# Kernel optimization log

Hardware: AMD Instinct MI355X
Metric: run time of the kernel (lower is better)

## Reference

```python
import jax, jax.numpy as jnp
import numpy as np

B, T, R = 512, 4096, 16


def setup_inputs() -> dict:
    key = jax.random.key(0)
    k1, k2, k3 = jax.random.split(key, 3)
    pred = jax.random.normal(k1, (B, T, R), dtype=jnp.float32)
    target = jax.random.normal(k2, (B, T, R), dtype=jnp.float32)
    # replicate_mask marks a contiguous prefix of valid replicates (matches
    # the original `pred[b, :, :n_valid]` slicing). Lengths in [0, R].
    lengths = jax.random.randint(k3, (B,), 0, R + 1)
    replicate_mask = (jnp.arange(R)[None, :] < lengths[:, None]).astype(jnp.float32)
    return {"pred": pred, "target": target, "replicate_mask": replicate_mask}


def _masked_var_unbiased(x, m, n_safe):
    # x: [B,T,R], m: [B,1,R], n_safe: [B,1] (clamped >= 2)
    mean = jnp.sum(x * m, axis=-1, keepdims=True) / n_safe[:, :, None]  # [B,T,1]
    sq = jnp.sum(((x - mean) ** 2) * m, axis=-1)  # [B,T]
    return sq / (n_safe - 1.0)  # unbiased (torch var default ddof=1)


def reference(pred, target, replicate_mask):
    weight = 0.1
    n = jnp.sum(replicate_mask, axis=-1)  # [B]
    n_safe = jnp.maximum(n, 2.0)[:, None]  # avoid div-by-zero; masked out below
    m = replicate_mask[:, None, :]  # [B,1,R]
    pred_var = _masked_var_unbiased(pred, m, n_safe)      # [B,T]
    target_var = _masked_var_unbiased(target, m, n_safe)  # [B,T]
    mse = jnp.mean((pred_var - target_var) ** 2, axis=-1)  # [B]
    valid = n > 1.0
    n_multi = jnp.sum(valid.astype(jnp.float32))
    total = jnp.sum(jnp.where(valid, mse, 0.0))
    loss = jnp.where(n_multi > 0, total / jnp.maximum(n_multi, 1.0), 0.0)
    return weight * loss
```

## Files before the change

### kernel.cpp

```cpp
#include <hip/hip_runtime.h>

#define B_DIM 512
#define T_DIM 4096
#define NSLOT 256
#define THREADS 256
#define ITER 8
#define QROWS (B_DIM * T_DIM * 4)
#define BLOCKS (QROWS / (THREADS * ITER))

__device__ __forceinline__ float hsum4(float4 v) { return (v.x + v.y) + (v.z + v.w); }

__device__ __forceinline__ float mdot(float4 x, float4 m) {
    return (x.x * m.x + x.y * m.y) + (x.z * m.z + x.w * m.w);
}

__device__ __forceinline__ float mdot2(float4 x, float4 m) {
    return (x.x * x.x * m.x + x.y * x.y * m.y) + (x.z * x.z * m.z + x.w * x.w * m.w);
}

__device__ __forceinline__ float qsum(float v) {
    int t = __builtin_amdgcn_update_dpp(0, __float_as_int(v), 0xB1, 0xF, 0xF, true);
    v += __int_as_float(t);
    t = __builtin_amdgcn_update_dpp(0, __float_as_int(v), 0x4E, 0xF, 0xF, true);
    v += __int_as_float(t);
    return v;
}

__global__ __launch_bounds__(THREADS, 4) void rcl_main(
    const float4* __restrict__ pred4, const float4* __restrict__ targ4,
    const float4* __restrict__ mask4, double* __restrict__ slots)
{
    const int tid  = threadIdx.x;
    const int b    = blockIdx.x >> 3;
    const int base = blockIdx.x * (THREADS * ITER);

    const float4 mv = mask4[(b << 2) + (tid & 3)];
    const float n = qsum(hsum4(mv));
    if (n <= 1.0f) return;

    const float inv = 1.0f / (n * (n - 1.0f));

    float csum = 0.0f;
#pragma unroll
    for (int i = 0; i < ITER; i++) {
        const int g = base + i * THREADS + tid;
        const float4 p = pred4[g];
        const float4 q = targ4[g];
        float sp  = qsum(mdot(p, mv));
        float sp2 = qsum(mdot2(p, mv));
        float sq  = qsum(mdot(q, mv));
        float sq2 = qsum(mdot2(q, mv));
        float d = ((n * sp2 - sp * sp) - (n * sq2 - sq * sq)) * inv;
        csum += d * d * 0.25f;
    }

    for (int off = 32; off > 0; off >>= 1)
        csum += __shfl_down(csum, off, 64);

    __shared__ float partial[THREADS / 64];
    const int w = tid >> 6;
    const int lane = tid & 63;
    if (lane == 0) partial[w] = csum;
    __syncthreads();
    if (tid == 0) {
        float s = (partial[0] + partial[1]) + (partial[2] + partial[3]);
        atomicAdd(&slots[blockIdx.x & (NSLOT - 1)], (double)s);
    }
}

__global__ __launch_bounds__(256) void rcl_final(
    const double* __restrict__ slots, const float4* __restrict__ mask4,
    float* __restrict__ out)
{
    __shared__ double dred[256];
    __shared__ float fred[256];
    const int t = threadIdx.x;

    double tot = slots[t];

    float cnt = 0.0f;
    for (int bb = t; bb < B_DIM; bb += 256) {
        const float4* mp = mask4 + (bb << 2);
        float nn = (hsum4(mp[0]) + hsum4(mp[1])) + (hsum4(mp[2]) + hsum4(mp[3]));
        cnt += (nn > 1.0f) ? 1.0f : 0.0f;
    }

    dred[t] = tot;
    fred[t] = cnt;
    __syncthreads();
    for (int s = 128; s > 0; s >>= 1) {
        if (t < s) { dred[t] += dred[t + s]; fred[t] += fred[t + s]; }
        __syncthreads();
    }
    if (t == 0) {
        double nm = (double)fred[0];
        out[0] = (nm > 0.0) ? (float)(0.1 * (dred[0] / ((double)T_DIM * nm))) : 0.0f;
    }
}

extern "C" void kernel_launch(void* const* d_in, const int* in_sizes, int n_in,
                              void* d_out, int out_size, void* d_ws, size_t ws_size,
                              hipStream_t stream) {
    const float4* pred4 = (const float4*)d_in[0];
    const float4* targ4 = (const float4*)d_in[1];
    const float4* mask4 = (const float4*)d_in[2];
    float* out = (float*)d_out;

    double* slots = (double*)d_ws;

    hipMemsetAsync(d_ws, 0, NSLOT * sizeof(double), stream);
    rcl_main<<<BLOCKS, THREADS, 0, stream>>>(pred4, targ4, mask4, slots);
    rcl_final<<<1, 256, 0, stream>>>(slots, mask4, out);
}
```

Before: 274.2 us.

## Stage inputs via direct global-to-LDS loads and drop atomics with per-block partials

Loads of pred and target now go straight from global memory into LDS through global_load_lds, all issued up front before a single wait, and are then read back from LDS for the reduction. The per-block double atomics into 256 slots and the memset are replaced by one plain store per block, which the final kernel sums. This aims to raise memory-level parallelism and remove the memset launch and atomic contention. In exchange it uses 64KB of LDS per block, which limits occupancy, and the launch-bounds occupancy hint is dropped.

```diff
diff --git a/kernel.cpp b/kernel.cpp
--- a/kernel.cpp
+++ b/kernel.cpp
@@ -2,11 +2,11 @@
 
 #define B_DIM 512
 #define T_DIM 4096
-#define NSLOT 256
 #define THREADS 256
-#define ITER 8
+#define NWAVE (THREADS / 64)
+#define KITER 8
 #define QROWS (B_DIM * T_DIM * 4)
-#define BLOCKS (QROWS / (THREADS * ITER))
+#define BLOCKS (QROWS / (THREADS * KITER))
 
 __device__ __forceinline__ float hsum4(float4 v) { return (v.x + v.y) + (v.z + v.w); }
 
@@ -26,26 +26,45 @@
     return v;
 }
 
-__global__ __launch_bounds__(THREADS, 4) void rcl_main(
+__device__ __forceinline__ void stage16(const float4* g, float4* l) {
+    __builtin_amdgcn_global_load_lds((const __attribute__((address_space(1))) void*)g,
+                                     (__attribute__((address_space(3))) void*)l, 16, 0, 0);
+}
+
+__global__ __launch_bounds__(THREADS) void rcl_main(
     const float4* __restrict__ pred4, const float4* __restrict__ targ4,
-    const float4* __restrict__ mask4, double* __restrict__ slots)
+    const float4* __restrict__ mask4, double* __restrict__ ws)
 {
+    __shared__ float4 sbuf[2][NWAVE][KITER][64];
+
     const int tid  = threadIdx.x;
+    const int w    = tid >> 6;
+    const int lane = tid & 63;
     const int b    = blockIdx.x >> 3;
-    const int base = blockIdx.x * (THREADS * ITER);
+    const int base = blockIdx.x * (THREADS * KITER);
 
     const float4 mv = mask4[(b << 2) + (tid & 3)];
     const float n = qsum(hsum4(mv));
-    if (n <= 1.0f) return;
+    if (n <= 1.0f) {
+        if (tid == 0) ws[blockIdx.x] = 0.0;
+        return;
+    }
+
+#pragma unroll
+    for (int k = 0; k < KITER; k++) {
+        const int g = base + (w * KITER + k) * 64 + lane;
+        stage16(&pred4[g], &sbuf[0][w][k][0]);
+        stage16(&targ4[g], &sbuf[1][w][k][0]);
+    }
+    asm volatile("s_waitcnt vmcnt(0)" ::: "memory");
+    __builtin_amdgcn_sched_barrier(0);
 
     const float inv = 1.0f / (n * (n - 1.0f));
-
     float csum = 0.0f;
 #pragma unroll
-    for (int i = 0; i < ITER; i++) {
-        const int g = base + i * THREADS + tid;
-        const float4 p = pred4[g];
-        const float4 q = targ4[g];
+    for (int k = 0; k < KITER; k++) {
+        const float4 p = sbuf[0][w][k][lane];
+        const float4 q = sbuf[1][w][k][lane];
         float sp  = qsum(mdot(p, mv));
         float sp2 = qsum(mdot2(p, mv));
         float sq  = qsum(mdot(q, mv));
@@ -57,26 +76,27 @@
     for (int off = 32; off > 0; off >>= 1)
         csum += __shfl_down(csum, off, 64);
 
-    __shared__ float partial[THREADS / 64];
-    const int w = tid >> 6;
-    const int lane = tid & 63;
+    __shared__ float partial[NWAVE];
     if (lane == 0) partial[w] = csum;
     __syncthreads();
     if (tid == 0) {
         float s = (partial[0] + partial[1]) + (partial[2] + partial[3]);
-        atomicAdd(&slots[blockIdx.x & (NSLOT - 1)], (double)s);
+        ws[blockIdx.x] = (double)s;
     }
 }
 
 __global__ __launch_bounds__(256) void rcl_final(
-    const double* __restrict__ slots, const float4* __restrict__ mask4,
+    const double* __restrict__ ws, const float4* __restrict__ mask4,
     float* __restrict__ out)
 {
     __shared__ double dred[256];
     __shared__ float fred[256];
     const int t = threadIdx.x;
 
-    double tot = slots[t];
+    double tot = 0.0;
+#pragma unroll
+    for (int j = 0; j < BLOCKS / 256; j++)
+        tot += ws[t + j * 256];
 
     float cnt = 0.0f;
     for (int bb = t; bb < B_DIM; bb += 256) {
@@ -106,9 +126,8 @@
     const float4* mask4 = (const float4*)d_in[2];
     float* out = (float*)d_out;
 
-    double* slots = (double*)d_ws;
+    double* ws = (double*)d_ws;
 
-    hipMemsetAsync(d_ws, 0, NSLOT * sizeof(double), stream);
-    rcl_main<<<BLOCKS, THREADS, 0, stream>>>(pred4, targ4, mask4, slots);
-    rcl_final<<<1, 256, 0, stream>>>(slots, mask4, out);
+    rcl_main<<<BLOCKS, THREADS, 0, stream>>>(pred4, targ4, mask4, ws);
+    rcl_final<<<1, 256, 0, stream>>>(ws, mask4, out);
 }
```

Measured after the change: 269.2 us. About the same (-1.8%).
